# Kernel optimization log

Hardware: AMD Instinct MI355X
Metric: run time of the kernel (lower is better)

Reference implementation:

```python
import jax, jax.numpy as jnp
import numpy as np

HEADS = 8
HEAD_DIM = 64
SCALE = HEAD_DIM ** -0.5


def setup_inputs() -> dict:
    key = jax.random.key(0)
    ks = jax.random.split(key, 5)
    d_model, inner = 1024, HEADS * HEAD_DIM  # 512
    x = jax.random.normal(ks[0], (2, 2048, d_model), dtype=jnp.float32)
    # torch Linear weights stored pre-transposed as [in, out]
    Wq = jax.random.normal(ks[1], (d_model, inner), dtype=jnp.float32) * (d_model ** -0.5)
    Wkv = jax.random.normal(ks[2], (d_model, 2 * inner), dtype=jnp.float32) * (d_model ** -0.5)
    Wo = jax.random.normal(ks[3], (inner, d_model), dtype=jnp.float32) * (inner ** -0.5)
    bo = jnp.zeros((d_model,), dtype=jnp.float32)
    return {"x": x, "Wq": Wq, "Wkv": Wkv, "Wo": Wo, "bo": bo}


def reference(x, Wq, Wkv, Wo, bo):
    b, n, _ = x.shape
    q = x @ Wq                       # [b, n, h*d]
    kv = x @ Wkv                     # [b, n, 2*h*d] (self-attention: context = x)
    k, v = jnp.split(kv, 2, axis=-1)

    def split_heads(t):
        return t.reshape(b, n, HEADS, HEAD_DIM).transpose(0, 2, 1, 3)  # [b, h, n, d]

    q, k, v = map(split_heads, (q, k, v))
    sim = jnp.einsum('bhid,bhjd->bhij', q, k) * SCALE  # [b, h, n, n]
    attn = jax.nn.softmax(sim, axis=-1)                # dropout p=0.0 -> identity
    out = jnp.einsum('bhij,bhjd->bhid', attn, v)       # [b, h, n, d]
    out = out.transpose(0, 2, 1, 3).reshape(b, n, HEADS * HEAD_DIM)
    return out @ Wo + bo
```

## Files before the change

kernel.cpp:

```cpp
#include <hip/hip_runtime.h>

typedef _Float16 f16;
typedef __attribute__((ext_vector_type(4))) _Float16 f16x4;
typedef __attribute__((ext_vector_type(8))) _Float16 f16x8;
typedef __attribute__((ext_vector_type(4))) float f32x4;

#define CEXP 0.18033688011112042f
#define QKB_LD 1056

__device__ __forceinline__ void gload16(const f16* g, f16* l) {
    __builtin_amdgcn_global_load_lds((const __attribute__((address_space(1))) void*)g,
                                     (__attribute__((address_space(3))) void*)l, 16, 0, 0);
}

__global__ __launch_bounds__(256) void conv_f32_f16_k(const float* __restrict__ in,
                                                      f16* __restrict__ out) {
    int idx = (blockIdx.x * 256 + threadIdx.x) * 8;
    float4 a = *(const float4*)(in + idx);
    float4 b = *(const float4*)(in + idx + 4);
    f16x8 o;
    o[0] = (f16)a.x; o[1] = (f16)a.y; o[2] = (f16)a.z; o[3] = (f16)a.w;
    o[4] = (f16)b.x; o[5] = (f16)b.y; o[6] = (f16)b.z; o[7] = (f16)b.w;
    *(f16x8*)(out + idx) = o;
}

__global__ __launch_bounds__(256) void transpose_conv_k(const float* __restrict__ in,
                                                        f16* __restrict__ out,
                                                        int N, int ldo, int row_off) {
    __shared__ float tile[32][33];
    int tx = threadIdx.x & 31, ty = threadIdx.x >> 5;
    int n0 = blockIdx.x * 32, k0 = blockIdx.y * 32;
#pragma unroll
    for (int j = 0; j < 4; j++)
        tile[ty + j * 8][tx] = in[(size_t)(k0 + ty + j * 8) * N + n0 + tx];
    __syncthreads();
#pragma unroll
    for (int j = 0; j < 4; j++)
        out[(size_t)(row_off + n0 + ty + j * 8) * ldo + k0 + tx] = (f16)tile[tx][ty + j * 8];
}

template <int MODE, int BN>
__global__ __launch_bounds__(256) void gemm_k(
    const f16* __restrict__ A, const f16* __restrict__ Bt,
    f16* __restrict__ Cqk, f16* __restrict__ Cvt,
    float* __restrict__ Cout, const float* __restrict__ bias,
    int K, int NTILES) {
    __shared__ __align__(16) f16 As[128 * 64];
    __shared__ __align__(16) f16 Bs[BN * 64];
    constexpr int MI = (BN == 128) ? 4 : 2;
    int bid = blockIdx.x;
    int nt = bid % NTILES, mt = bid / NTILES;
    int m0 = mt * 128, n0 = nt * BN;
    int tid = threadIdx.x;
    int lane = tid & 63, w = tid >> 6;
    int rowBase = (BN == 128) ? (w >> 1) * 64 : w * 32;
    int colBase = (BN == 128) ? (w & 1) * 64 : 0;
    int lr = lane & 15, lg = lane >> 4;
    int rowL = lane >> 3;
    int colL = (lane & 7) * 8;
    int bRow0 = (BN == 128) ? w * 32 : w * 16;
    const f16* aSrc = A + (size_t)(m0 + w * 32 + rowL) * K + colL;
    const f16* bSrc = Bt + (size_t)(n0 + bRow0 + rowL) * K + colL;
    f32x4 acc[MI][4] = {};

    for (int k0 = 0; k0 < K; k0 += 64) {
#pragma unroll
        for (int j = 0; j < 4; j++)
            gload16(aSrc + k0 + (size_t)(j * 8) * K, &As[(w * 32 + j * 8) * 64]);
#pragma unroll
        for (int j = 0; j < (BN == 128 ? 4 : 2); j++)
            gload16(bSrc + k0 + (size_t)(j * 8) * K, &Bs[(bRow0 + j * 8) * 64]);
        __syncthreads();
#pragma unroll
        for (int ks = 0; ks < 2; ks++) {
            f16x8 af[MI], bf[4];
#pragma unroll
            for (int i = 0; i < MI; i++)
                af[i] = *(const f16x8*)(&As[(rowBase + i * 16 + lr) * 64 + ks * 32 + lg * 8]);
#pragma unroll
            for (int j = 0; j < 4; j++)
                bf[j] = *(const f16x8*)(&Bs[(colBase + j * 16 + lr) * 64 + ks * 32 + lg * 8]);
#pragma unroll
            for (int i = 0; i < MI; i++)
#pragma unroll
                for (int j = 0; j < 4; j++)
                    acc[i][j] = __builtin_amdgcn_mfma_f32_16x16x32_f16(af[i], bf[j], acc[i][j], 0, 0, 0);
        }
        __syncthreads();
    }

#pragma unroll
    for (int i = 0; i < MI; i++) {
#pragma unroll
        for (int j = 0; j < 4; j++) {
            int row = m0 + rowBase + i * 16 + lg * 4;
            int col = n0 + colBase + j * 16 + lr;
            if (MODE == 1) {
                float bv = bias[col];
#pragma unroll
                for (int r = 0; r < 4; r++)
                    Cout[(size_t)(row + r) * 1024 + col] = acc[i][j][r] + bv;
            } else {
                if (col < 1024) {
                    float sc = (col < 512) ? CEXP : 1.0f;
#pragma unroll
                    for (int r = 0; r < 4; r++)
                        Cqk[(size_t)(row + r) * QKB_LD + col] = (f16)(acc[i][j][r] * sc);
                } else {
                    int c = col - 1024;
                    int hh = c >> 6, d = c & 63;
                    int bb = row >> 11, n = row & 2047;
                    int pr = bb * 8 + hh;
                    int tt = n >> 6, kvl = n & 63;
                    int kg = kvl >> 4, lga = (kvl >> 2) & 3;
                    int dgp = d >> 5, dh = (d >> 4) & 1, lra = d & 15;
                    f16x4 ov;
#pragma unroll
                    for (int r = 0; r < 4; r++) ov[r] = (f16)acc[i][j][r];
                    size_t idx = ((((size_t)(pr * 32 + tt) * 4 + kg) * 2 + dgp) * 64
                                  + lga * 16 + lra) * 8 + dh * 4;
                    *(f16x4*)(Cvt + idx) = ov;
                }
            }
        }
    }
}

__global__ __launch_bounds__(512, 4) void attn_k(const f16* __restrict__ qkb,
                                                 const f16* __restrict__ vt2,
                                                 f16* __restrict__ ao) {
    __shared__ __align__(16) f16 Ks[2][3 * 4096];
    __shared__ __align__(16) f16 Vs[2][2 * 4096];

    int bid = blockIdx.x;
    int xcd = bid & 7;
    int pair = xcd * 2 + ((bid >> 3) & 1);
    int qblk = bid >> 4;
    int b = pair >> 3, h = pair & 7;
    int tid = threadIdx.x;
    int lane = tid & 63, w = tid >> 6;
    int half = w >> 2, wl = w & 3;
    int lr = lane & 15, lg = lane >> 4;
    int q0 = qblk * 64 + wl * 16;

    const f16* qb = qkb + (size_t)b * 2048 * QKB_LD + h * 64;
    const f16* kb = qb + 512;

    f16x8 qf0 = *(const f16x8*)(qb + (size_t)(q0 + lr) * QKB_LD + lg * 8);
    f16x8 qf1 = *(const f16x8*)(qb + (size_t)(q0 + lr) * QKB_LD + 32 + lg * 8);

    int srcCol = (((lane & 7) ^ (lane >> 3)) << 3);
    int rowL = lane >> 3;
    const f16* ksrc = kb + (size_t)(half * 1024 + wl * 16 + rowL) * QKB_LD + srcCol;
    const f16* vsrc = vt2 + ((size_t)(pair * 32 + half * 16) * 8 + 2 * wl) * 512 + lane * 8;

    auto stageK = [&](int buf, int tt) {
        f16* dst = &Ks[half][buf * 4096 + (wl * 16) * 64];
        gload16(ksrc + (size_t)(tt * 64) * QKB_LD, dst);
        gload16(ksrc + (size_t)(tt * 64 + 8) * QKB_LD, dst + 8 * 64);
    };
    auto stageV = [&](int buf, int tt) {
        const f16* s = vsrc + (size_t)tt * 4096;
        f16* dst = &Vs[half][buf * 4096 + (2 * wl) * 512];
        gload16(s, dst);
        gload16(s + 512, dst + 512);
    };

    stageK(0, 0); stageV(0, 0); stageK(1, 1);
    __syncthreads();

    int kOffA = (lg * 8) ^ ((lr & 7) << 3);

    f32x4 acc[4] = {};
    float m = -INFINITY, lp = 0.f;
    f32x4 sA[4], sB[4];

    {
        __builtin_amdgcn_s_setprio(1);
#pragma unroll
        for (int kg = 0; kg < 4; kg++) {
            const f16* krow = &Ks[half][(kg * 16 + lr) * 64];
            f16x8 ka0 = *(const f16x8*)(krow + kOffA);
            f16x8 ka1 = *(const f16x8*)(krow + (kOffA ^ 32));
            f32x4 z = {};
            z = __builtin_amdgcn_mfma_f32_16x16x32_f16(ka0, qf0, z, 0, 0, 0);
            sA[kg] = __builtin_amdgcn_mfma_f32_16x16x32_f16(ka1, qf1, z, 0, 0, 0);
        }
        __builtin_amdgcn_s_setprio(0);
    }

    auto body = [&](f32x4 (&sCur)[4], f32x4 (&sNxt)[4], int t) {
        if (t <= 13) stageK((t + 2) % 3, t + 2);
        if (t <= 14) stageV((t + 1) & 1, t + 1);

        if (t < 15) {
            const f16* kbuf = &Ks[half][((t + 1) % 3) * 4096];
            __builtin_amdgcn_s_setprio(1);
#pragma unroll
            for (int kg = 0; kg < 4; kg++) {
                const f16* krow = kbuf + (kg * 16 + lr) * 64;
                f16x8 ka0 = *(const f16x8*)(krow + kOffA);
                f16x8 ka1 = *(const f16x8*)(krow + (kOffA ^ 32));
                f32x4 z = {};
                z = __builtin_amdgcn_mfma_f32_16x16x32_f16(ka0, qf0, z, 0, 0, 0);
                sNxt[kg] = __builtin_amdgcn_mfma_f32_16x16x32_f16(ka1, qf1, z, 0, 0, 0);
            }
            __builtin_amdgcn_s_setprio(0);
        }

        float x0 = fmaxf(fmaxf(sCur[0][0], sCur[0][1]), fmaxf(sCur[0][2], sCur[0][3]));
        float x1 = fmaxf(fmaxf(sCur[1][0], sCur[1][1]), fmaxf(sCur[1][2], sCur[1][3]));
        float x2 = fmaxf(fmaxf(sCur[2][0], sCur[2][1]), fmaxf(sCur[2][2], sCur[2][3]));
        float x3 = fmaxf(fmaxf(sCur[3][0], sCur[3][1]), fmaxf(sCur[3][2], sCur[3][3]));
        float ownmx = fmaxf(fmaxf(x0, x1), fmaxf(x2, x3));
        if (!__all(ownmx - m <= 8.f)) {
            float mx = fmaxf(ownmx, __shfl_xor(ownmx, 16, 64));
            mx = fmaxf(mx, __shfl_xor(mx, 32, 64));
            float mn = fmaxf(m, mx);
            float alpha = __builtin_amdgcn_exp2f(m - mn);
            m = mn;
            lp *= alpha;
#pragma unroll
            for (int dg = 0; dg < 4; dg++)
#pragma unroll
                for (int r = 0; r < 4; r++) acc[dg][r] *= alpha;
        }
        f16x4 pf[4];
#pragma unroll
        for (int kg = 0; kg < 4; kg++) {
            float p0 = __builtin_amdgcn_exp2f(sCur[kg][0] - m);
            float p1 = __builtin_amdgcn_exp2f(sCur[kg][1] - m);
            float p2 = __builtin_amdgcn_exp2f(sCur[kg][2] - m);
            float p3 = __builtin_amdgcn_exp2f(sCur[kg][3] - m);
            pf[kg][0] = (f16)p0; pf[kg][1] = (f16)p1;
            pf[kg][2] = (f16)p2; pf[kg][3] = (f16)p3;
            lp += (p0 + p1) + (p2 + p3);
        }

        const f16* vl = &Vs[half][(t & 1) * 4096] + lane * 8;
        __builtin_amdgcn_s_setprio(1);
#pragma unroll
        for (int kg = 0; kg < 4; kg++)
#pragma unroll
            for (int dgp = 0; dgp < 2; dgp++) {
                f16x8 vv = *(const f16x8*)(vl + (kg * 2 + dgp) * 512);
                f16x4 vlo = __builtin_shufflevector(vv, vv, 0, 1, 2, 3);
                f16x4 vhi = __builtin_shufflevector(vv, vv, 4, 5, 6, 7);
                acc[dgp * 2]     = __builtin_amdgcn_mfma_f32_16x16x16f16(vlo, pf[kg], acc[dgp * 2], 0, 0, 0);
                acc[dgp * 2 + 1] = __builtin_amdgcn_mfma_f32_16x16x16f16(vhi, pf[kg], acc[dgp * 2 + 1], 0, 0, 0);
            }
        __builtin_amdgcn_s_setprio(0);

        if (t < 15) __syncthreads();
    };

    for (int u = 0; u < 8; u++) {
        body(sA, sB, 2 * u);
        body(sB, sA, 2 * u + 1);
    }

    lp += __shfl_xor(lp, 16, 64);
    lp += __shfl_xor(lp, 32, 64);
    __syncthreads();
    float* mO = (float*)&Ks[0][0];
    float* mL = mO + 4 * 64 * 16;
    float* mM = mL + 4 * 64;
    if (half == 1) {
#pragma unroll
        for (int dg = 0; dg < 4; dg++)
            *(f32x4*)&mO[(wl * 64 + lane) * 16 + dg * 4] = acc[dg];
        mL[wl * 64 + lane] = lp;
        mM[wl * 64 + lane] = m;
    }
    __syncthreads();
    if (half == 0) {
        float mP = mM[wl * 64 + lane];
        float lpP = mL[wl * 64 + lane];
        float M = fmaxf(m, mP);
        float a = __builtin_amdgcn_exp2f(m - M);
        float c = __builtin_amdgcn_exp2f(mP - M);
        float inv = 1.f / (lp * a + lpP * c);
#pragma unroll
        for (int dg = 0; dg < 4; dg++) {
            f32x4 oP = *(const f32x4*)&mO[(wl * 64 + lane) * 16 + dg * 4];
            f16x4 ov;
#pragma unroll
            for (int r = 0; r < 4; r++)
                ov[r] = (f16)((acc[dg][r] * a + oP[r] * c) * inv);
            *(f16x4*)(ao + (size_t)(b * 2048 + q0 + lr) * 512 + h * 64 + dg * 16 + lg * 4) = ov;
        }
    }
}

extern "C" void kernel_launch(void* const* d_in, const int* in_sizes, int n_in,
                              void* d_out, int out_size, void* d_ws, size_t ws_size,
                              hipStream_t stream) {
    const float* x   = (const float*)d_in[0];
    const float* Wq  = (const float*)d_in[1];
    const float* Wkv = (const float*)d_in[2];
    const float* Wo  = (const float*)d_in[3];
    const float* bo  = (const float*)d_in[4];
    float* out = (float*)d_out;

    f16* xb    = (f16*)d_ws;
    f16* wqkvT = xb + 4096 * 1024;
    f16* woT   = wqkvT + 1536 * 1024;
    f16* qkb   = woT + 1024 * 512;
    f16* vtb2  = qkb + 4096 * QKB_LD;
    f16* ao    = vtb2 + 16 * 32 * 4096;

    conv_f32_f16_k<<<2048, 256, 0, stream>>>(x, xb);
    transpose_conv_k<<<dim3(16, 32), 256, 0, stream>>>(Wq, wqkvT, 512, 1024, 0);
    transpose_conv_k<<<dim3(32, 32), 256, 0, stream>>>(Wkv, wqkvT, 1024, 1024, 512);
    transpose_conv_k<<<dim3(32, 16), 256, 0, stream>>>(Wo, woT, 1024, 512, 0);

    gemm_k<0, 64><<<32 * 24, 256, 0, stream>>>(xb, wqkvT, qkb, vtb2, nullptr, nullptr, 1024, 24);
    attn_k<<<512, 512, 0, stream>>>(qkb, vtb2, ao);
    gemm_k<1, 128><<<32 * 8, 256, 0, stream>>>(ao, woT, nullptr, nullptr, out, bo, 512, 8);
}
```

Before: 90.08 us.

## Load V fragments directly from global and deepen K LDS pipeline to four buffers

V tiles are no longer staged through LDS. Each wave now reads its V fragments straight from global memory into registers at the start of each iteration. The LDS that held V is reused to make the K staging ring four buffers deep instead of three. The full __syncthreads is replaced by a manual s_waitcnt vmcnt plus s_barrier, so outstanding K prefetches can stay in flight across iterations. This is meant to cut LDS traffic and sync cost, but it adds register pressure (eight f16x8 per lane) and exposes global-load latency for V inside each iteration. The hand-counted vmcnt values also have to account for the V loads that are now in flight alongside the K prefetches.

```diff
diff --git a/kernel.cpp b/kernel.cpp
--- a/kernel.cpp
+++ b/kernel.cpp
@@ -129,8 +129,7 @@
 __global__ __launch_bounds__(512, 4) void attn_k(const f16* __restrict__ qkb,
                                                  const f16* __restrict__ vt2,
                                                  f16* __restrict__ ao) {
-    __shared__ __align__(16) f16 Ks[2][3 * 4096];
-    __shared__ __align__(16) f16 Vs[2][2 * 4096];
+    __shared__ __align__(16) f16 Ks[2][4 * 4096];
 
     int bid = blockIdx.x;
     int xcd = bid & 7;
@@ -152,22 +151,18 @@
     int srcCol = (((lane & 7) ^ (lane >> 3)) << 3);
     int rowL = lane >> 3;
     const f16* ksrc = kb + (size_t)(half * 1024 + wl * 16 + rowL) * QKB_LD + srcCol;
-    const f16* vsrc = vt2 + ((size_t)(pair * 32 + half * 16) * 8 + 2 * wl) * 512 + lane * 8;
+    const f16* vbase = vt2 + ((size_t)pair * 32) * 4096 + lane * 8;
 
     auto stageK = [&](int buf, int tt) {
         f16* dst = &Ks[half][buf * 4096 + (wl * 16) * 64];
         gload16(ksrc + (size_t)(tt * 64) * QKB_LD, dst);
         gload16(ksrc + (size_t)(tt * 64 + 8) * QKB_LD, dst + 8 * 64);
     };
-    auto stageV = [&](int buf, int tt) {
-        const f16* s = vsrc + (size_t)tt * 4096;
-        f16* dst = &Vs[half][buf * 4096 + (2 * wl) * 512];
-        gload16(s, dst);
-        gload16(s + 512, dst + 512);
-    };
-
-    stageK(0, 0); stageV(0, 0); stageK(1, 1);
-    __syncthreads();
+
+    stageK(0, 0); stageK(1, 1); stageK(2, 2);
+    asm volatile("s_waitcnt vmcnt(2)" ::: "memory");
+    __builtin_amdgcn_s_barrier();
+    asm volatile("" ::: "memory");
 
     int kOffA = (lg * 8) ^ ((lr & 7) << 3);
 
@@ -190,11 +185,15 @@
     }
 
     auto body = [&](f32x4 (&sCur)[4], f32x4 (&sNxt)[4], int t) {
-        if (t <= 13) stageK((t + 2) % 3, t + 2);
-        if (t <= 14) stageV((t + 1) & 1, t + 1);
+        const f16* vl = vbase + (size_t)(half * 16 + t) * 4096;
+        f16x8 vv[8];
+#pragma unroll
+        for (int i = 0; i < 8; i++) vv[i] = *(const f16x8*)(vl + i * 512);
+
+        if (t <= 12) stageK((t + 3) & 3, t + 3);
 
         if (t < 15) {
-            const f16* kbuf = &Ks[half][((t + 1) % 3) * 4096];
+            const f16* kbuf = &Ks[half][((t + 1) & 3) * 4096];
             __builtin_amdgcn_s_setprio(1);
 #pragma unroll
             for (int kg = 0; kg < 4; kg++) {
@@ -237,21 +236,25 @@
             lp += (p0 + p1) + (p2 + p3);
         }
 
-        const f16* vl = &Vs[half][(t & 1) * 4096] + lane * 8;
         __builtin_amdgcn_s_setprio(1);
 #pragma unroll
         for (int kg = 0; kg < 4; kg++)
 #pragma unroll
             for (int dgp = 0; dgp < 2; dgp++) {
-                f16x8 vv = *(const f16x8*)(vl + (kg * 2 + dgp) * 512);
-                f16x4 vlo = __builtin_shufflevector(vv, vv, 0, 1, 2, 3);
-                f16x4 vhi = __builtin_shufflevector(vv, vv, 4, 5, 6, 7);
+                f16x8 vx = vv[kg * 2 + dgp];
+                f16x4 vlo = __builtin_shufflevector(vx, vx, 0, 1, 2, 3);
+                f16x4 vhi = __builtin_shufflevector(vx, vx, 4, 5, 6, 7);
                 acc[dgp * 2]     = __builtin_amdgcn_mfma_f32_16x16x16f16(vlo, pf[kg], acc[dgp * 2], 0, 0, 0);
                 acc[dgp * 2 + 1] = __builtin_amdgcn_mfma_f32_16x16x16f16(vhi, pf[kg], acc[dgp * 2 + 1], 0, 0, 0);
             }
         __builtin_amdgcn_s_setprio(0);
 
-        if (t < 15) __syncthreads();
+        if (t <= 12)      { asm volatile("s_waitcnt vmcnt(2)" ::: "memory"); }
+        else if (t == 13) { asm volatile("s_waitcnt vmcnt(0)" ::: "memory"); }
+        if (t < 15) {
+            __builtin_amdgcn_s_barrier();
+            asm volatile("" ::: "memory");
+        }
     };
 
     for (int u = 0; u < 8; u++) {
```

After: 92.34 us. 1.03x slower.
